# Kernel optimization log

Hardware: AMD Instinct MI355X
Metric: run time of the kernel (lower is better)

Reference implementation:

```python
import jax, jax.numpy as jnp
import numpy as np
import math

B, S, D, H = 1, 2048, 2048, 16
DH, DHID, DKER = 128, 256, 128  # dim_head, dim_hid, dim_ker


def _uniform(k, shape, a):
    return jax.random.uniform(k, shape, jnp.float32, -a, a)


def setup_inputs() -> dict:
    key = jax.random.key(0)
    ks = jax.random.split(key, 14)
    a1 = math.sqrt(6.0 / (DH + DHID))
    a2 = math.sqrt(6.0 / (DKER + DHID))
    a3 = math.sqrt(6.0 / (2 * DKER))
    return {
        "x_t": jax.random.normal(ks[0], (B, S, D), jnp.float32),
        "q": jax.random.normal(ks[1], (B, S, D), jnp.float32),
        "k": jax.random.normal(ks[2], (B, S, D), jnp.float32),
        "v": jax.random.normal(ks[3], (B, S, D), jnp.float32),
        "lr_attn_mask": jax.random.bernoulli(ks[4], 0.5, (B, H, S, S)),
        "sparse_norms_lse": jax.random.normal(ks[5], (B, H, S, 1), jnp.float32),
        "sparse_attn_weights": jax.random.normal(ks[6], (B, H, S, S), jnp.float32),
        "lambda_constant": 0,
        "kernel_q_mat1": _uniform(ks[7], (H, DH, DHID), a1),
        "kernel_k_mat1": _uniform(ks[8], (H, DH, DHID), a1),
        "kernel_q_mat2": _uniform(ks[9], (H, DHID, DKER), a2),
        "kernel_k_mat2": _uniform(ks[10], (H, DHID, DKER), a2),
        "interaction_k": _uniform(ks[11], (H, DKER, DKER), a3),
        "scalingD": jnp.full((1, H, 1, DKER), 1e-4, jnp.float32),
        "scalingD2": jnp.full((1, H, 1, DKER), 1e-4, jnp.float32),
    }


def _gelu(x):
    return jax.nn.gelu(x, approximate=False)  # matches torch F.gelu default


def reference(x_t, q, k, v, lr_attn_mask, sparse_norms_lse, sparse_attn_weights,
              lambda_constant, kernel_q_mat1, kernel_k_mat1, kernel_q_mat2,
              kernel_k_mat2, interaction_k, scalingD, scalingD2):
    Bq, Sq, Dq = q.shape
    dh = Dq // H
    # [B,S,D] -> [B,H,S,dh]
    qh = q.reshape(Bq, Sq, H, dh).transpose(0, 2, 1, 3)
    kh = k.reshape(Bq, Sq, H, dh).transpose(0, 2, 1, 3)
    vh = v.reshape(Bq, Sq, H, dh).transpose(0, 2, 1, 3)

    # per-head two-layer feature maps (dropout is identity at eval)
    qf = _gelu(jnp.einsum('bhsd,hde->bhse', qh, kernel_q_mat1))
    qf = _gelu(jnp.einsum('bhse,hef->bhsf', qf, kernel_q_mat2))
    kf = _gelu(jnp.einsum('bhsd,hde->bhse', kh, kernel_k_mat1))
    kf = jnp.abs(scalingD) * _gelu(jnp.einsum('bhse,hef->bhsf', kf, kernel_k_mat2))
    kf = kf + jnp.einsum('bhse,hef->bhsf', kf, interaction_k) * scalingD2

    # masked non-negative kernel scores [B,H,S,S]
    scores = jnp.einsum('bhse,bhte->bhst', jnp.abs(qf), jnp.abs(kf))
    m = lr_attn_mask.astype(scores.dtype)
    scores = m * scores

    lr_norms_lse = jnp.log(scores.sum(axis=-1, keepdims=True) + 1e-6)
    norm_factor_lse = jnp.logaddexp(lr_norms_lse, sparse_norms_lse)

    logits = jnp.log(scores + 1e-6) * m + (1.0 - m) * sparse_attn_weights
    attn = jnp.exp(logits - norm_factor_lse)

    out = jnp.einsum('bhst,bhtd->bhsd', attn, vh)
    return out.transpose(0, 2, 1, 3).reshape(Bq, Sq, Dq)
```

## Files before the change

kernel.cpp:

```cpp
#include <hip/hip_runtime.h>
#include <hip/hip_bf16.h>
#include <math.h>

#define H_    16
#define S_    2048
#define D_    2048
#define DH_   128
#define DHID_ 256
#define DKER_ 128

typedef __attribute__((ext_vector_type(8))) short short8v;
typedef __attribute__((ext_vector_type(4))) float float4v;

static __device__ __forceinline__ short f2bf(float x){
  union { float f; unsigned u; } v; v.f = x;
  unsigned r = v.u + 0x7fffu + ((v.u >> 16) & 1u);
  return (short)(r >> 16);
}
static __device__ __forceinline__ float gelu_f(float x){
  return 0.5f * x * (1.0f + erff(x * 0.70710678118654752440f));
}
static __device__ __forceinline__ float4v mfma16(short8v a, short8v b, float4v c){
  return __builtin_amdgcn_mfma_f32_16x16x32_bf16(a, b, c, 0, 0, 0);
}
static __device__ __forceinline__ unsigned cvtpk(float lo, float hi){
  unsigned d;
  asm("v_cvt_pk_bf16_f32 %0, %1, %2" : "=v"(d) : "v"(lo), "v"(hi));
  return d;
}
static __device__ __forceinline__ void glds16(const void* g, void* l){
  __builtin_amdgcn_global_load_lds(
      (const __attribute__((address_space(1))) void*)g,
      (__attribute__((address_space(3))) void*)l, 16, 0, 0);
}

__global__ void detect_mask_kernel(const unsigned int* mw, int* flag){
  int t = threadIdx.x;
  int bin = 1, f32ok = 1, odd0 = 1;
  for (int i = t; i < 1024; i += 256){
    unsigned w = mw[i];
    if (w > 1u) bin = 0;
    if (w != 0u && w != 0x3F800000u) f32ok = 0;
    if ((i & 1) && w != 0u) odd0 = 0;
  }
  __shared__ int sb, sf, so;
  if (t == 0){ sb = 1; sf = 1; so = 1; }
  __syncthreads();
  if (!bin)  atomicAnd(&sb, 0);
  if (!f32ok) atomicAnd(&sf, 0);
  if (!odd0) atomicAnd(&so, 0);
  __syncthreads();
  if (t == 0) *flag = sb ? (so ? 3 : 0) : (sf ? 2 : 1);
}

__global__ __launch_bounds__(256) void prep_kernel(
    const void* __restrict__ mask, const int* __restrict__ flagp,
    unsigned* __restrict__ MP,
    const float* __restrict__ w1q, short* __restrict__ W1qT,
    const float* __restrict__ w1k, short* __restrict__ W1kT,
    const float* __restrict__ w2q, short* __restrict__ W2qT,
    const float* __restrict__ w2k, short* __restrict__ W2kT,
    const float* __restrict__ ik,  short* __restrict__ IKT,
    const float* __restrict__ v,   short* __restrict__ V2){
  __shared__ float tile[32][33];
  int b = blockIdx.x;
  int tid = threadIdx.x;

  if (b < 8192){
    int flag = *flagp;
    size_t w = (size_t)b * 256 + tid;
    size_t base = w * 32;
    unsigned bits = 0;
    if (flag == 0){
      const int* m = (const int*)mask;
      #pragma unroll
      for (int i = 0; i < 32; ++i) bits |= (m[base + i] != 0 ? 1u : 0u) << i;
    } else if (flag == 1){
      const unsigned char* m = (const unsigned char*)mask;
      #pragma unroll
      for (int i = 0; i < 32; ++i) bits |= (m[base + i] != 0 ? 1u : 0u) << i;
    } else if (flag == 2){
      const float* m = (const float*)mask;
      #pragma unroll
      for (int i = 0; i < 32; ++i) bits |= (m[base + i] != 0.0f ? 1u : 0u) << i;
    } else {
      const int* m = (const int*)mask;
      #pragma unroll
      for (int i = 0; i < 32; ++i) bits |= (m[2*(base + i)] != 0 ? 1u : 0u) << i;
    }
    MP[w] = bits;
    return;
  }
  b -= 8192;
  if (b < 2048){
    int h = b >> 7, bx = b & 127;
    int d = tid & 127, oct = tid >> 7;
    int t8 = bx * 2 + oct;
    const float* src = v + (size_t)(t8 * 8) * D_ + h * DH_ + d;
    short8v o;
    #pragma unroll
    for (int j = 0; j < 8; ++j) o[j] = f2bf(src[(size_t)j * D_]);
    *(short8v*)(V2 + (((size_t)h * (S_/8) + t8) * DH_ + d) * 8) = o;
    return;
  }
  b -= 2048;
  const float* src; short* dst; int R, C, bx, by, h;
  if (b < 512){        src = w1q; dst = W1qT; R = DH_;  C = DHID_;
                       bx = b & 7; by = (b >> 3) & 3; h = b >> 5; }
  else if (b < 1024){  b -= 512;  src = w1k; dst = W1kT; R = DH_;  C = DHID_;
                       bx = b & 7; by = (b >> 3) & 3; h = b >> 5; }
  else if (b < 1536){  b -= 1024; src = w2q; dst = W2qT; R = DHID_; C = DKER_;
                       bx = b & 3; by = (b >> 2) & 7; h = b >> 5; }
  else if (b < 2048){  b -= 1536; src = w2k; dst = W2kT; R = DHID_; C = DKER_;
                       bx = b & 3; by = (b >> 2) & 7; h = b >> 5; }
  else {               b -= 2048; src = ik;  dst = IKT;  R = DKER_; C = DKER_;
                       bx = b & 3; by = (b >> 2) & 3; h = b >> 4; }
  int tx = tid & 31, ty = tid >> 5;
  int c0 = bx * 32, r0 = by * 32;
  const float* s = src + (size_t)h * R * C;
  short* d = dst + (size_t)h * R * C;
  #pragma unroll
  for (int i = 0; i < 32; i += 8)
    tile[ty + i][tx] = s[(size_t)(r0 + ty + i) * C + (c0 + tx)];
  __syncthreads();
  #pragma unroll
  for (int i = 0; i < 32; i += 8)
    d[(size_t)(c0 + ty + i) * R + (r0 + tx)] = f2bf(tile[tx][ty + i]);
}

__global__ __launch_bounds__(256) void featq_kernel(const float* __restrict__ X,
    const short* __restrict__ W1T, const short* __restrict__ W2T,
    short* __restrict__ QF){
  __shared__ __align__(16) short yls[4][16][264];
  int h = blockIdx.y;
  int lane = threadIdx.x & 63, warp = threadIdx.x >> 6;
  int s0 = (blockIdx.x * 4 + warp) * 16;
  int col = lane & 15, rg = lane >> 4;
  short8v a[4];
  {
    const float* xr = X + (size_t)(s0 + col) * D_ + h * DH_;
    #pragma unroll
    for (int kb = 0; kb < 4; ++kb){
      int k0 = kb * 32 + rg * 8;
      float4v x0 = *(const float4v*)(xr + k0);
      float4v x1 = *(const float4v*)(xr + k0 + 4);
      short8v t;
      t[0]=f2bf(x0[0]); t[1]=f2bf(x0[1]); t[2]=f2bf(x0[2]); t[3]=f2bf(x0[3]);
      t[4]=f2bf(x1[0]); t[5]=f2bf(x1[1]); t[6]=f2bf(x1[2]); t[7]=f2bf(x1[3]);
      a[kb] = t;
    }
  }
  const short* wbase = W1T + (size_t)h * DHID_ * DH_;
  #pragma unroll
  for (int j = 0; j < 16; ++j){
    int n = j * 16;
    float4v c = {0.f, 0.f, 0.f, 0.f};
    const short* wr = wbase + (size_t)(n + col) * DH_ + rg * 8;
    #pragma unroll
    for (int kb = 0; kb < 4; ++kb)
      c = mfma16(a[kb], *(const short8v*)(wr + kb * 32), c);
    #pragma unroll
    for (int r = 0; r < 4; ++r)
      yls[warp][rg * 4 + r][n + col] = f2bf(gelu_f(c[r]));
  }
  __syncthreads();
  short8v a2[8];
  #pragma unroll
  for (int kb = 0; kb < 8; ++kb)
    a2[kb] = *(const short8v*)(&yls[warp][col][kb * 32 + rg * 8]);
  const short* wb2 = W2T + (size_t)h * DKER_ * DHID_;
  short* qb = QF + ((size_t)h * S_ + s0) * DKER_;
  #pragma unroll
  for (int j = 0; j < 8; ++j){
    int n = j * 16;
    float4v c = {0.f, 0.f, 0.f, 0.f};
    const short* wr = wb2 + (size_t)(n + col) * DHID_ + rg * 8;
    #pragma unroll
    for (int kb = 0; kb < 8; ++kb)
      c = mfma16(a2[kb], *(const short8v*)(wr + kb * 32), c);
    #pragma unroll
    for (int r = 0; r < 4; ++r)
      qb[(size_t)(rg * 4 + r) * DKER_ + n + col] = f2bf(fabsf(gelu_f(c[r])));
  }
}

__global__ __launch_bounds__(256) void featk_kernel(const float* __restrict__ X,
    const short* __restrict__ W1T, const short* __restrict__ W2T,
    const short* __restrict__ IKT, const float* __restrict__ sD,
    const float* __restrict__ sD2, short* __restrict__ KF){
  __shared__ __align__(16) short yls[4][16][264];
  int h = blockIdx.y;
  int lane = threadIdx.x & 63, warp = threadIdx.x >> 6;
  int s0 = (blockIdx.x * 4 + warp) * 16;
  int col = lane & 15, rg = lane >> 4;
  short8v a[4];
  {
    const float* xr = X + (size_t)(s0 + col) * D_ + h * DH_;
    #pragma unroll
    for (int kb = 0; kb < 4; ++kb){
      int k0 = kb * 32 + rg * 8;
      float4v x0 = *(const float4v*)(xr + k0);
      float4v x1 = *(const float4v*)(xr + k0 + 4);
      short8v t;
      t[0]=f2bf(x0[0]); t[1]=f2bf(x0[1]); t[2]=f2bf(x0[2]); t[3]=f2bf(x0[3]);
      t[4]=f2bf(x1[0]); t[5]=f2bf(x1[1]); t[6]=f2bf(x1[2]); t[7]=f2bf(x1[3]);
      a[kb] = t;
    }
  }
  const short* wbase = W1T + (size_t)h * DHID_ * DH_;
  #pragma unroll
  for (int j = 0; j < 16; ++j){
    int n = j * 16;
    float4v c = {0.f, 0.f, 0.f, 0.f};
    const short* wr = wbase + (size_t)(n + col) * DH_ + rg * 8;
    #pragma unroll
    for (int kb = 0; kb < 4; ++kb)
      c = mfma16(a[kb], *(const short8v*)(wr + kb * 32), c);
    #pragma unroll
    for (int r = 0; r < 4; ++r)
      yls[warp][rg * 4 + r][n + col] = f2bf(gelu_f(c[r]));
  }
  __syncthreads();
  short8v a2[8];
  #pragma unroll
  for (int kb = 0; kb < 8; ++kb)
    a2[kb] = *(const short8v*)(&yls[warp][col][kb * 32 + rg * 8]);
  const short* wb2 = W2T + (size_t)h * DKER_ * DHID_;
  float kf0[8][4];
  #pragma unroll
  for (int j = 0; j < 8; ++j){
    int n = j * 16;
    float4v c = {0.f, 0.f, 0.f, 0.f};
    const short* wr = wb2 + (size_t)(n + col) * DHID_ + rg * 8;
    #pragma unroll
    for (int kb = 0; kb < 8; ++kb)
      c = mfma16(a2[kb], *(const short8v*)(wr + kb * 32), c);
    float sc = fabsf(sD[h * DKER_ + n + col]);
    #pragma unroll
    for (int r = 0; r < 4; ++r) kf0[j][r] = sc * gelu_f(c[r]);
  }
  __syncthreads();
  #pragma unroll
  for (int j = 0; j < 8; ++j)
    #pragma unroll
    for (int r = 0; r < 4; ++r)
      yls[warp][rg * 4 + r][j * 16 + col] = f2bf(kf0[j][r]);
  __syncthreads();
  short8v pa[4];
  #pragma unroll
  for (int kb = 0; kb < 4; ++kb)
    pa[kb] = *(const short8v*)(&yls[warp][col][kb * 32 + rg * 8]);
  const short* ib = IKT + (size_t)h * DKER_ * DKER_;
  short* ko = KF + ((size_t)h * S_ + s0) * DKER_;
  #pragma unroll
  for (int j = 0; j < 8; ++j){
    int n = j * 16;
    float4v c = {0.f, 0.f, 0.f, 0.f};
    const short* ir = ib + (size_t)(n + col) * DKER_ + rg * 8;
    #pragma unroll
    for (int kb = 0; kb < 4; ++kb)
      c = mfma16(pa[kb], *(const short8v*)(ir + kb * 32), c);
    float s2 = sD2[h * DKER_ + n + col];
    #pragma unroll
    for (int r = 0; r < 4; ++r)
      ko[(size_t)(rg * 4 + r) * DKER_ + n + col] = f2bf(fabsf(kf0[j][r] + c[r] * s2));
  }
}

__global__ __launch_bounds__(256, 4) void main_attn_kernel(
    const short* __restrict__ QF, const short* __restrict__ KF,
    const short* __restrict__ V2, const unsigned* __restrict__ MP,
    const float* __restrict__ SW, const float* __restrict__ LSE,
    float* __restrict__ OUT, float* __restrict__ PU, float* __restrict__ PR,
    int nsplit){
  __shared__ __align__(16) short kbuf[2][4096];
  __shared__ __align__(16) short vbuf[2][4096];
  int lane = threadIdx.x & 63, warp = threadIdx.x >> 6;
  int flat = blockIdx.y * 32 + blockIdx.x;
  int nf = (flat & 7) * 64 + (flat >> 3);
  int sblk = nf & 31, h = nf >> 5;
  int split = blockIdx.z;
  int niter = (S_ / 32) / nsplit;
  int tbase = split * (S_ / nsplit);
  int s0 = (sblk * 4 + warp) * 16;
  int col = lane & 15, rg = lane >> 4;

  short8v qa[4];
  const short* qr = QF + ((size_t)h * S_ + s0 + col) * DKER_ + rg * 8;
  #pragma unroll
  for (int kb = 0; kb < 4; ++kb) qa[kb] = *(const short8v*)(qr + kb * 32);

  float4v acc[8];
  #pragma unroll
  for (int j = 0; j < 8; ++j) acc[j] = (float4v){0.f, 0.f, 0.f, 0.f};
  float rs = 0.f;

  const char* kf_base = (const char*)(KF + ((size_t)h * S_ + tbase) * DKER_);
  const char* v2_base = (const char*)(V2 + ((size_t)h * (S_/8) + (tbase >> 3)) * DH_ * 8);
  int c0 = warp * 64 + lane, c1 = c0 + 256;
  int kg0 = (c0 * 16) ^ (((c0 >> 4) & 7) << 4);
  int kg1 = (c1 * 16) ^ (((c1 >> 4) & 7) << 4);
  int vg0 = c0 * 16, vg1 = c1 * 16;
  int lds_lo = warp * 512, lds_hi = 2048 + warp * 512;

  const float* swrow = SW + ((size_t)h * S_ + s0 + col) * S_ + tbase + rg * 4;
  const unsigned* mpr = MP + ((size_t)h * S_ + s0 + col) * (S_ / 32) + (tbase >> 5);

  {
    const char* kt = kf_base; const char* vt = v2_base;
    glds16(kt + kg0, &kbuf[0][lds_lo]);
    glds16(kt + kg1, &kbuf[0][lds_hi]);
    glds16(vt + vg0, &vbuf[0][lds_lo]);
    glds16(vt + vg1, &vbuf[0][lds_hi]);
  }
  __syncthreads();

  int swz = (col & 7) << 4;
  int rowb0 = col * 256 + rg * 16;
  int ga = col + ((2 * (rg & 1)) << 4);
  int gb = ga + 16;
  bool hi = (rg >= 2);

  for (int ti = 0; ti < niter; ++ti){
    int cur = ti & 1;
    if (ti + 1 < niter){
      const char* kt = kf_base + (size_t)(ti + 1) * 8192;
      const char* vt = v2_base + (size_t)(ti + 1) * 8192;
      glds16(kt + kg0, &kbuf[cur ^ 1][lds_lo]);
      glds16(kt + kg1, &kbuf[cur ^ 1][lds_hi]);
      glds16(vt + vg0, &vbuf[cur ^ 1][lds_lo]);
      glds16(vt + vg1, &vbuf[cur ^ 1][lds_hi]);
    }
    const char* kbp = (const char*)&kbuf[cur][0];
    const char* vbp = (const char*)&vbuf[cur][0];

    float4v q0 = {0.f,0.f,0.f,0.f}, q1 = {0.f,0.f,0.f,0.f};
    #pragma unroll
    for (int kk = 0; kk < 4; ++kk){
      short8v a0 = *(const short8v*)(kbp + ((rowb0 + kk * 64) ^ swz));
      short8v a1 = *(const short8v*)(kbp + ((rowb0 + 4096 + kk * 64) ^ swz));
      q0 = mfma16(a0, qa[kk], q0);
      q1 = mfma16(a1, qa[kk], q1);
    }

    const float* swp = swrow + ti * 32;
    float4v sv0 = *(const float4v*)swp;
    float4v sv1 = *(const float4v*)(swp + 16);
    unsigned mw = mpr[ti];
    float p0[4], p1[4];
    #pragma unroll
    for (int r = 0; r < 4; ++r){
      bool m0 = (mw >> (rg * 4 + r)) & 1u;
      bool m1 = (mw >> (16 + rg * 4 + r)) & 1u;
      p0[r] = m0 ? (q0[r] + 1e-6f) : expf(sv0[r]);
      p1[r] = m1 ? (q1[r] + 1e-6f) : expf(sv1[r]);
      if (m0) rs += q0[r];
      if (m1) rs += q1[r];
    }
    unsigned k00 = cvtpk(p0[0], p0[1]), k01 = cvtpk(p0[2], p0[3]);
    unsigned k10 = cvtpk(p1[0], p1[1]), k11 = cvtpk(p1[2], p1[3]);
    unsigned a0 = __shfl((int)k00, ga), b0 = __shfl((int)k10, ga);
    unsigned a1 = __shfl((int)k01, ga), b1 = __shfl((int)k11, ga);
    unsigned a2 = __shfl((int)k00, gb), b2 = __shfl((int)k10, gb);
    unsigned a3 = __shfl((int)k01, gb), b3 = __shfl((int)k11, gb);
    union { unsigned u[4]; short8v v8; } pw;
    pw.u[0] = hi ? b0 : a0; pw.u[1] = hi ? b1 : a1;
    pw.u[2] = hi ? b2 : a2; pw.u[3] = hi ? b3 : a3;
    short8v pa = pw.v8;

    #pragma unroll
    for (int j = 0; j < 8; ++j){
      short8v vf = *(const short8v*)(vbp + rg * 2048 + (j * 16 + col) * 16);
      acc[j] = mfma16(pa, vf, acc[j]);
    }
    __syncthreads();
  }

  rs += __shfl_xor(rs, 16);
  rs += __shfl_xor(rs, 32);

  if (nsplit == 1){
    float a = logf(rs + 1e-6f);
    float b = LSE[h * S_ + s0 + col];
    float mx = fmaxf(a, b);
    float sc_col = expf(-(mx + log1pf(expf(-fabsf(a - b)))));
    float scale[4];
    #pragma unroll
    for (int r = 0; r < 4; ++r) scale[r] = __shfl(sc_col, rg * 4 + r);
    float* ob = OUT + (size_t)s0 * D_ + h * DH_;
    #pragma unroll
    for (int j = 0; j < 8; ++j)
      #pragma unroll
      for (int r = 0; r < 4; ++r)
        ob[(size_t)(rg * 4 + r) * D_ + j * 16 + col] = acc[j][r] * scale[r];
  } else {
    float* pu = PU + (((size_t)split * H_ + h) * S_ + s0) * DH_;
    #pragma unroll
    for (int j = 0; j < 8; ++j)
      #pragma unroll
      for (int r = 0; r < 4; ++r)
        pu[(size_t)(rg * 4 + r) * DH_ + j * 16 + col] = acc[j][r];
    if (lane < 16)
      PR[((size_t)split * H_ + h) * S_ + s0 + lane] = rs;
  }
}

__global__ __launch_bounds__(256) void reduce_kernel(
    const float* __restrict__ PU, const float* __restrict__ PR,
    const float* __restrict__ LSE, float* __restrict__ OUT, int nsplit){
  size_t gid = (size_t)blockIdx.x * 256 + threadIdx.x;
  int d4 = (int)(gid & 31);
  int s  = (int)(gid >> 5) & (S_ - 1);
  int h  = (int)(gid >> 16);
  float4v u = {0.f, 0.f, 0.f, 0.f};
  float rr = 0.f;
  for (int i = 0; i < nsplit; ++i){
    u  += *(const float4v*)(PU + (((size_t)i * H_ + h) * S_ + s) * DH_ + d4 * 4);
    rr += PR[((size_t)i * H_ + h) * S_ + s];
  }
  float a = logf(rr + 1e-6f);
  float b = LSE[h * S_ + s];
  float mx = fmaxf(a, b);
  float sc = expf(-(mx + log1pf(expf(-fabsf(a - b)))));
  *(float4v*)(OUT + (size_t)s * D_ + h * DH_ + d4 * 4) = u * sc;
}

extern "C" void kernel_launch(void* const* d_in, const int* in_sizes, int n_in,
                              void* d_out, int out_size, void* d_ws, size_t ws_size,
                              hipStream_t stream){
  (void)in_sizes; (void)n_in; (void)out_size;
  const float* q   = (const float*)d_in[1];
  const float* k   = (const float*)d_in[2];
  const float* v   = (const float*)d_in[3];
  const void*  msk = d_in[4];
  const float* lse = (const float*)d_in[5];
  const float* sw  = (const float*)d_in[6];
  const float* w1q = (const float*)d_in[8];
  const float* w1k = (const float*)d_in[9];
  const float* w2q = (const float*)d_in[10];
  const float* w2k = (const float*)d_in[11];
  const float* ik  = (const float*)d_in[12];
  const float* sD  = (const float*)d_in[13];
  const float* sD2 = (const float*)d_in[14];
  float* out = (float*)d_out;

  char* ws = (char*)d_ws;
  size_t o = 0;
  int*   flag = (int*)(ws);            o += 256;
  short* W1qT = (short*)(ws + o);      o += (size_t)H_ * DHID_ * DH_ * 2;
  short* W1kT = (short*)(ws + o);      o += (size_t)H_ * DHID_ * DH_ * 2;
  short* W2qT = (short*)(ws + o);      o += (size_t)H_ * DKER_ * DHID_ * 2;
  short* W2kT = (short*)(ws + o);      o += (size_t)H_ * DKER_ * DHID_ * 2;
  short* IKT  = (short*)(ws + o);      o += (size_t)H_ * DKER_ * DKER_ * 2;
  short* V2   = (short*)(ws + o);      o += (size_t)S_ * D_ * 2;
  short* QFb  = (short*)(ws + o);      o += (size_t)H_ * S_ * DKER_ * 2;
  short* KFb  = (short*)(ws + o);      o += (size_t)H_ * S_ * DKER_ * 2;
  unsigned* MP = (unsigned*)(ws + o);  o += (size_t)H_ * S_ * (S_/32) * 4;

  size_t per_split = (size_t)H_ * S_ * DH_ * 4 + (size_t)H_ * S_ * 4;
  int nsplit = (ws_size >= o + 2 * per_split) ? 2 : 1;
  float* PU = (float*)(ws + o);
  float* PR = PU + (size_t)nsplit * H_ * S_ * DH_;

  detect_mask_kernel<<<1, 256, 0, stream>>>((const unsigned int*)msk, flag);
  prep_kernel<<<12544, 256, 0, stream>>>(msk, flag, MP,
      w1q, W1qT, w1k, W1kT, w2q, W2qT, w2k, W2kT, ik, IKT, v, V2);

  featq_kernel<<<dim3(S_/64, H_), 256, 0, stream>>>(q, W1qT, W2qT, QFb);
  featk_kernel<<<dim3(S_/64, H_), 256, 0, stream>>>(k, W1kT, W2kT, IKT, sD, sD2, KFb);

  main_attn_kernel<<<dim3(32, 16, nsplit), 256, 0, stream>>>(
      QFb, KFb, V2, MP, sw, lse, out, PU, PR, nsplit);
  if (nsplit > 1)
    reduce_kernel<<<(H_*S_*DH_/4)/256, 256, 0, stream>>>(PU, PR, lse, out, nsplit);
}
```

Measured before the change: 267.3 us.

## Split key range across two warp groups in-block, reduce via LDS, drop reduce kernel

The attention kernel now runs 512 threads per block. Two groups of four warps each process half of the key sequence with their own LDS double buffers. Their partial accumulators and row sums are combined through shared memory before normalization, replacing the global split-K partial buffers and the separate reduce kernel. This removes the global write and read of the partial outputs and one launch, at the cost of 64KB of LDS per block, a 512-thread block and an extra barrier-based reduction. It also switches the exp on sparse weights to the fast __expf intrinsic.

```diff
diff --git a/kernel.cpp b/kernel.cpp
--- a/kernel.cpp
+++ b/kernel.cpp
@@ -267,23 +267,24 @@
   }
 }
 
-__global__ __launch_bounds__(256, 4) void main_attn_kernel(
+__global__ __launch_bounds__(512, 4) void main_attn_kernel(
     const short* __restrict__ QF, const short* __restrict__ KF,
     const short* __restrict__ V2, const unsigned* __restrict__ MP,
     const float* __restrict__ SW, const float* __restrict__ LSE,
-    float* __restrict__ OUT, float* __restrict__ PU, float* __restrict__ PR,
-    int nsplit){
-  __shared__ __align__(16) short kbuf[2][4096];
-  __shared__ __align__(16) short vbuf[2][4096];
-  int lane = threadIdx.x & 63, warp = threadIdx.x >> 6;
+    float* __restrict__ OUT){
+  __shared__ __align__(16) char smem[65536];
+  int tid = threadIdx.x;
+  int lane = tid & 63, warp = tid >> 6;
+  int hf = warp >> 2, w4 = warp & 3;
   int flat = blockIdx.y * 32 + blockIdx.x;
   int nf = (flat & 7) * 64 + (flat >> 3);
   int sblk = nf & 31, h = nf >> 5;
-  int split = blockIdx.z;
-  int niter = (S_ / 32) / nsplit;
-  int tbase = split * (S_ / nsplit);
-  int s0 = (sblk * 4 + warp) * 16;
+  int tbase = hf * (S_ / 2);
+  int s0 = (sblk * 4 + w4) * 16;
   int col = lane & 15, rg = lane >> 4;
+
+  short* kbuf = (short*)(smem + hf * 32768);
+  short* vbuf = (short*)(smem + hf * 32768 + 16384);
 
   short8v qa[4];
   const short* qr = QF + ((size_t)h * S_ + s0 + col) * DKER_ + rg * 8;
@@ -297,21 +298,20 @@
 
   const char* kf_base = (const char*)(KF + ((size_t)h * S_ + tbase) * DKER_);
   const char* v2_base = (const char*)(V2 + ((size_t)h * (S_/8) + (tbase >> 3)) * DH_ * 8);
-  int c0 = warp * 64 + lane, c1 = c0 + 256;
+  int c0 = w4 * 64 + lane, c1 = c0 + 256;
   int kg0 = (c0 * 16) ^ (((c0 >> 4) & 7) << 4);
   int kg1 = (c1 * 16) ^ (((c1 >> 4) & 7) << 4);
   int vg0 = c0 * 16, vg1 = c1 * 16;
-  int lds_lo = warp * 512, lds_hi = 2048 + warp * 512;
+  int lds_lo = w4 * 512, lds_hi = 2048 + w4 * 512;
 
   const float* swrow = SW + ((size_t)h * S_ + s0 + col) * S_ + tbase + rg * 4;
   const unsigned* mpr = MP + ((size_t)h * S_ + s0 + col) * (S_ / 32) + (tbase >> 5);
 
   {
-    const char* kt = kf_base; const char* vt = v2_base;
-    glds16(kt + kg0, &kbuf[0][lds_lo]);
-    glds16(kt + kg1, &kbuf[0][lds_hi]);
-    glds16(vt + vg0, &vbuf[0][lds_lo]);
-    glds16(vt + vg1, &vbuf[0][lds_hi]);
+    glds16(kf_base + kg0, &kbuf[lds_lo]);
+    glds16(kf_base + kg1, &kbuf[lds_hi]);
+    glds16(v2_base + vg0, &vbuf[lds_lo]);
+    glds16(v2_base + vg1, &vbuf[lds_hi]);
   }
   __syncthreads();
 
@@ -320,19 +320,20 @@
   int ga = col + ((2 * (rg & 1)) << 4);
   int gb = ga + 16;
   bool hi = (rg >= 2);
-
-  for (int ti = 0; ti < niter; ++ti){
+  const int NITER = (S_ / 2) / 32;
+
+  for (int ti = 0; ti < NITER; ++ti){
     int cur = ti & 1;
-    if (ti + 1 < niter){
+    if (ti + 1 < NITER){
       const char* kt = kf_base + (size_t)(ti + 1) * 8192;
       const char* vt = v2_base + (size_t)(ti + 1) * 8192;
-      glds16(kt + kg0, &kbuf[cur ^ 1][lds_lo]);
-      glds16(kt + kg1, &kbuf[cur ^ 1][lds_hi]);
-      glds16(vt + vg0, &vbuf[cur ^ 1][lds_lo]);
-      glds16(vt + vg1, &vbuf[cur ^ 1][lds_hi]);
-    }
-    const char* kbp = (const char*)&kbuf[cur][0];
-    const char* vbp = (const char*)&vbuf[cur][0];
+      glds16(kt + kg0, &kbuf[(cur ^ 1) * 4096 + lds_lo]);
+      glds16(kt + kg1, &kbuf[(cur ^ 1) * 4096 + lds_hi]);
+      glds16(vt + vg0, &vbuf[(cur ^ 1) * 4096 + lds_lo]);
+      glds16(vt + vg1, &vbuf[(cur ^ 1) * 4096 + lds_hi]);
+    }
+    const char* kbp = (const char*)kbuf + cur * 8192;
+    const char* vbp = (const char*)vbuf + cur * 8192;
 
     float4v q0 = {0.f,0.f,0.f,0.f}, q1 = {0.f,0.f,0.f,0.f};
     #pragma unroll
@@ -352,8 +353,8 @@
     for (int r = 0; r < 4; ++r){
       bool m0 = (mw >> (rg * 4 + r)) & 1u;
       bool m1 = (mw >> (16 + rg * 4 + r)) & 1u;
-      p0[r] = m0 ? (q0[r] + 1e-6f) : expf(sv0[r]);
-      p1[r] = m1 ? (q1[r] + 1e-6f) : expf(sv1[r]);
+      p0[r] = m0 ? (q0[r] + 1e-6f) : __expf(sv0[r]);
+      p1[r] = m1 ? (q1[r] + 1e-6f) : __expf(sv1[r]);
       if (m0) rs += q0[r];
       if (m1) rs += q1[r];
     }
@@ -379,7 +380,28 @@
   rs += __shfl_xor(rs, 16);
   rs += __shfl_xor(rs, 32);
 
-  if (nsplit == 1){
+  __syncthreads();
+  float* cb = (float*)smem;
+  float* rb = (float*)(smem + 32768);
+  if (hf == 1){
+    float* cw = cb + (size_t)w4 * 16 * 128;
+    #pragma unroll
+    for (int j = 0; j < 8; ++j)
+      #pragma unroll
+      for (int r = 0; r < 4; ++r)
+        cw[(size_t)(rg * 4 + r) * 128 + j * 16 + col] = acc[j][r];
+    if (lane < 16) rb[w4 * 16 + lane] = rs;
+  }
+  __syncthreads();
+  if (hf == 0){
+    float* cw = cb + (size_t)w4 * 16 * 128;
+    #pragma unroll
+    for (int j = 0; j < 8; ++j)
+      #pragma unroll
+      for (int r = 0; r < 4; ++r)
+        acc[j][r] += cw[(size_t)(rg * 4 + r) * 128 + j * 16 + col];
+    rs += rb[w4 * 16 + col];
+
     float a = logf(rs + 1e-6f);
     float b = LSE[h * S_ + s0 + col];
     float mx = fmaxf(a, b);
@@ -393,42 +415,13 @@
       #pragma unroll
       for (int r = 0; r < 4; ++r)
         ob[(size_t)(rg * 4 + r) * D_ + j * 16 + col] = acc[j][r] * scale[r];
-  } else {
-    float* pu = PU + (((size_t)split * H_ + h) * S_ + s0) * DH_;
-    #pragma unroll
-    for (int j = 0; j < 8; ++j)
-      #pragma unroll
-      for (int r = 0; r < 4; ++r)
-        pu[(size_t)(rg * 4 + r) * DH_ + j * 16 + col] = acc[j][r];
-    if (lane < 16)
-      PR[((size_t)split * H_ + h) * S_ + s0 + lane] = rs;
-  }
-}
-
-__global__ __launch_bounds__(256) void reduce_kernel(
-    const float* __restrict__ PU, const float* __restrict__ PR,
-    const float* __restrict__ LSE, float* __restrict__ OUT, int nsplit){
-  size_t gid = (size_t)blockIdx.x * 256 + threadIdx.x;
-  int d4 = (int)(gid & 31);
-  int s  = (int)(gid >> 5) & (S_ - 1);
-  int h  = (int)(gid >> 16);
-  float4v u = {0.f, 0.f, 0.f, 0.f};
-  float rr = 0.f;
-  for (int i = 0; i < nsplit; ++i){
-    u  += *(const float4v*)(PU + (((size_t)i * H_ + h) * S_ + s) * DH_ + d4 * 4);
-    rr += PR[((size_t)i * H_ + h) * S_ + s];
-  }
-  float a = logf(rr + 1e-6f);
-  float b = LSE[h * S_ + s];
-  float mx = fmaxf(a, b);
-  float sc = expf(-(mx + log1pf(expf(-fabsf(a - b)))));
-  *(float4v*)(OUT + (size_t)s * D_ + h * DH_ + d4 * 4) = u * sc;
+  }
 }
 
 extern "C" void kernel_launch(void* const* d_in, const int* in_sizes, int n_in,
                               void* d_out, int out_size, void* d_ws, size_t ws_size,
                               hipStream_t stream){
-  (void)in_sizes; (void)n_in; (void)out_size;
+  (void)in_sizes; (void)n_in; (void)out_size; (void)ws_size;
   const float* q   = (const float*)d_in[1];
   const float* k   = (const float*)d_in[2];
   const float* v   = (const float*)d_in[3];
@@ -457,11 +450,6 @@
   short* KFb  = (short*)(ws + o);      o += (size_t)H_ * S_ * DKER_ * 2;
   unsigned* MP = (unsigned*)(ws + o);  o += (size_t)H_ * S_ * (S_/32) * 4;
 
-  size_t per_split = (size_t)H_ * S_ * DH_ * 4 + (size_t)H_ * S_ * 4;
-  int nsplit = (ws_size >= o + 2 * per_split) ? 2 : 1;
-  float* PU = (float*)(ws + o);
-  float* PR = PU + (size_t)nsplit * H_ * S_ * DH_;
-
   detect_mask_kernel<<<1, 256, 0, stream>>>((const unsigned int*)msk, flag);
   prep_kernel<<<12544, 256, 0, stream>>>(msk, flag, MP,
       w1q, W1qT, w1k, W1kT, w2q, W2qT, w2k, W2kT, ik, IKT, v, V2);
@@ -469,8 +457,6 @@
   featq_kernel<<<dim3(S_/64, H_), 256, 0, stream>>>(q, W1qT, W2qT, QFb);
   featk_kernel<<<dim3(S_/64, H_), 256, 0, stream>>>(k, W1kT, W2kT, IKT, sD, sD2, KFb);
 
-  main_attn_kernel<<<dim3(32, 16, nsplit), 256, 0, stream>>>(
-      QFb, KFb, V2, MP, sw, lse, out, PU, PR, nsplit);
-  if (nsplit > 1)
-    reduce_kernel<<<(H_*S_*DH_/4)/256, 256, 0, stream>>>(PU, PR, lse, out, nsplit);
-}
+  main_attn_kernel<<<dim3(32, 16), 512, 0, stream>>>(
+      QFb, KFb, V2, MP, sw, lse, out);
+}
```

After: 246.5 us. 7.8% less time.
